# Kernel tuning notes

Hardware: AMD Instinct MI355X
Metric: run time of the kernel (lower is better)

The kernel has to match this reference:

```python
import jax, jax.numpy as jnp
import numpy as np

HEADS = 16
KEY_SIZE = 64
HEAD_SIZE = 64
D_MODEL = 1024
MASK_BIG = 1e12


def setup_inputs() -> dict:
    key = jax.random.key(0)
    ks = jax.random.split(key, 16)
    B, S, D = 4, 2048, D_MODEL
    qk_dim = HEADS * KEY_SIZE
    out_dim = HEADS * HEAD_SIZE
    s = 0.02
    return {
        'q': jax.random.normal(ks[0], (B, S, D), jnp.float32),
        'k': jax.random.normal(ks[1], (B, S, D), jnp.float32),
        'v': jax.random.normal(ks[2], (B, S, D), jnp.float32),
        'q_mask': jax.random.randint(ks[3], (B, S), 0, 2, jnp.int32),
        'v_mask': jax.random.randint(ks[4], (B, S), 0, 2, jnp.int32),
        'Wq': jax.random.normal(ks[5], (D, qk_dim), jnp.float32) * s,
        'bq': jnp.zeros((qk_dim,), jnp.float32),
        'Wk': jax.random.normal(ks[6], (D, qk_dim), jnp.float32) * s,
        'bk': jnp.zeros((qk_dim,), jnp.float32),
        'Wv': jax.random.normal(ks[7], (D, out_dim), jnp.float32) * s,
        'bv': jnp.zeros((out_dim,), jnp.float32),
        'Wo': jax.random.normal(ks[8], (out_dim, out_dim), jnp.float32) * s,
        'bo': jnp.zeros((out_dim,), jnp.float32),
    }


def reference(q, k, v, q_mask, v_mask, Wq, bq, Wk, bk, Wv, bv, Wo, bo):
    B, Sq, _ = q.shape
    Sk = k.shape[1]
    # projections -> [B, H, S, d]
    qw = (q @ Wq + bq).reshape(B, Sq, HEADS, KEY_SIZE).transpose(0, 2, 1, 3)
    kw = (k @ Wk + bk).reshape(B, Sk, HEADS, KEY_SIZE).transpose(0, 2, 1, 3)
    vw = (v @ Wv + bv).reshape(B, Sk, HEADS, HEAD_SIZE).transpose(0, 2, 1, 3)
    # scaled dot-product scores [B, H, Sq, Sk]
    a = jnp.einsum('bhqd,bhkd->bhqk', qw, kw) / np.sqrt(KEY_SIZE).astype(np.float32)
    # v_mask: additive -inf-like penalty on padded keys (mode=1, axis=-1)
    vm = v_mask.astype(a.dtype)[:, None, None, :]
    a = a - (1.0 - vm) * MASK_BIG
    # a_mask=True: causal mask (mask future positions)
    causal = jnp.tril(jnp.ones((Sq, Sk), a.dtype))
    a = a - (1.0 - causal) * MASK_BIG
    a = jax.nn.softmax(a, axis=-1)
    # attention output [B, Sq, H*head_size]
    o = jnp.einsum('bhqk,bhkd->bhqd', a, vw).transpose(0, 2, 1, 3).reshape(B, Sq, HEADS * HEAD_SIZE)
    o = o @ Wo + bo
    # q_mask: multiplicative zeroing of padded query outputs (mode=0, axis=1)
    o = o * q_mask.astype(o.dtype)[:, :, None]
    return o
```

## Files before the change

### kernel.cpp

```cpp
#include <hip/hip_runtime.h>
#include <hip/hip_bf16.h>

typedef __attribute__((ext_vector_type(8))) short v8s;
typedef __attribute__((ext_vector_type(4))) float v4f;
typedef __attribute__((ext_vector_type(16))) float v16f;
typedef __attribute__((ext_vector_type(4))) unsigned v4u;

#define S_LEN 2048
#define NB 4
#define NH 16
#define LOG2E 1.4426950408889634f
#define CMASK 1443109011456.0f
#define DEFER_THR 11.55f

__device__ __forceinline__ short f2bf(float f) {
    __hip_bfloat16 h = __float2bfloat16(f);
    union { __hip_bfloat16 h; short s; } u; u.h = h; return u.s;
}

__device__ __forceinline__ unsigned cvtpk(float lo, float hi) {
    unsigned r;
    asm("v_cvt_pk_bf16_f32 %0, %1, %2" : "=v"(r) : "v"(lo), "v"(hi));
    return r;
}

__device__ __forceinline__ void async16(void* lds, const void* g) {
    __builtin_amdgcn_global_load_lds(
        (const __attribute__((address_space(1))) unsigned int*)g,
        (__attribute__((address_space(3))) unsigned int*)lds, 16, 0, 0);
}

#define MFMA16(a, b, c) __builtin_amdgcn_mfma_f32_16x16x32_bf16((a), (b), (c), 0, 0, 0)
#define MFMA32(a, b, c) __builtin_amdgcn_mfma_f32_32x32x16_bf16((a), (b), (c), 0, 0, 0)

__global__ __launch_bounds__(256) void convert_all(const float* __restrict__ q,
                                                   const float* __restrict__ k,
                                                   const float* __restrict__ v,
                                                   short* __restrict__ Xq,
                                                   short* __restrict__ Xk,
                                                   short* __restrict__ Xv,
                                                   float* __restrict__ outz) {
    if (blockIdx.y == 3) {
        size_t i = ((size_t)blockIdx.x * 256 + threadIdx.x) * 8;
        float4 z4 = {0.f, 0.f, 0.f, 0.f};
        *(float4*)(outz + i) = z4;
        *(float4*)(outz + i + 4) = z4;
        return;
    }
    const float* in = (blockIdx.y == 0) ? q : (blockIdx.y == 1) ? k : v;
    short* out = (blockIdx.y == 0) ? Xq : (blockIdx.y == 1) ? Xk : Xv;
    size_t i = ((size_t)blockIdx.x * 256 + threadIdx.x) * 8;
    float4 a = *(const float4*)(in + i);
    float4 b = *(const float4*)(in + i + 4);
    v8s o;
    o[0] = f2bf(a.x); o[1] = f2bf(a.y); o[2] = f2bf(a.z); o[3] = f2bf(a.w);
    o[4] = f2bf(b.x); o[5] = f2bf(b.y); o[6] = f2bf(b.z); o[7] = f2bf(b.w);
    *(v8s*)(out + i) = o;
}

__global__ __launch_bounds__(256) void build_pen(const int* __restrict__ vm,
                                                 short* __restrict__ penC) {
    int i = blockIdx.x * 256 + threadIdx.x;
    penC[i] = vm[i] ? (short)0 : f2bf(-CMASK);
}

__global__ __launch_bounds__(256) void compact_qmask(const int* __restrict__ qm,
                                                     int* __restrict__ idx,
                                                     int* __restrict__ nq) {
    const int b = blockIdx.x;
    const int* m = qm + b * S_LEN;
    int* ib = idx + b * S_LEN;
    __shared__ int cnt[256];
    const int t = threadIdx.x;
    int loc[8], c = 0;
#pragma unroll
    for (int i = 0; i < 8; ++i) { int s = t * 8 + i; if (m[s]) loc[c++] = s; }
    cnt[t] = c;
    __syncthreads();
    for (int d = 1; d < 256; d <<= 1) {
        int v = (t >= d) ? cnt[t - d] : 0;
        __syncthreads();
        cnt[t] += v;
        __syncthreads();
    }
    int off = cnt[t] - c;
    for (int i = 0; i < c; ++i) ib[off + i] = loc[i];
    if (t == 255) nq[b] = cnt[255];
}

__global__ __launch_bounds__(256) void transpose_all(const float* __restrict__ Wq,
                                                     const float* __restrict__ Wk,
                                                     const float* __restrict__ Wv,
                                                     const float* __restrict__ Wo,
                                                     short* __restrict__ WTq,
                                                     short* __restrict__ WTk,
                                                     short* __restrict__ WTv,
                                                     short* __restrict__ WTo) {
    const int z = blockIdx.z;
    const float* W = (z == 0) ? Wq : (z == 1) ? Wk : (z == 2) ? Wv : Wo;
    short* WT = (z == 0) ? WTq : (z == 1) ? WTk : (z == 2) ? WTv : WTo;
    __shared__ float tile[32][33];
    int k0 = blockIdx.x * 32, n0 = blockIdx.y * 32;
    int tx = threadIdx.x & 31, ty = threadIdx.x >> 5;
#pragma unroll
    for (int i = 0; i < 4; ++i)
        tile[ty + i * 8][tx] = W[(size_t)(k0 + ty + i * 8) * 1024 + n0 + tx];
    __syncthreads();
#pragma unroll
    for (int i = 0; i < 4; ++i)
        WT[(size_t)(n0 + ty + i * 8) * 1024 + k0 + tx] = f2bf(tile[tx][ty + i * 8]);
}

__global__ __launch_bounds__(256)
void proj_all(const short* __restrict__ Xk, const short* __restrict__ Xv,
              const short* __restrict__ Xq,
              const short* __restrict__ WTk, const short* __restrict__ WTv,
              const short* __restrict__ WTq,
              const float* __restrict__ bk, const float* __restrict__ bv,
              const float* __restrict__ bq,
              const int* __restrict__ idx, const int* __restrict__ nq,
              short* __restrict__ KW, short* __restrict__ VT,
              short* __restrict__ QW) {
    __shared__ short As[128 * 64];
    __shared__ short Bs[128 * 64];
    const int tid = threadIdx.x;
    const int l = tid & 63, w = tid >> 6;
    const int g = l >> 4, ql = l & 15;
    const int z = blockIdx.z;
    const int n0 = blockIdx.x * 128;
    const int by = blockIdx.y;
    const int wr = w >> 1, wc = w & 1;

    int b = 0, m0 = by * 128, m0c = 0, nqv = 0;
    const int* idxb = nullptr;
    if (z == 2) {
        if (by >= 36) return;
        b = by / 9; m0c = (by % 9) * 128;
        nqv = nq[b];
        if (m0c >= nqv) return;
        idxb = idx + b * S_LEN;
    }
    const short* A  = (z == 0) ? Xk : (z == 1) ? Xv : Xq;
    const short* BT = (z == 0) ? WTk : (z == 1) ? WTv : WTq;
    const float* bias = (z == 0) ? bk : (z == 1) ? bv : bq;

    int arow[4];
#pragma unroll
    for (int i = 0; i < 4; ++i) {
        int row = (i * 256 + tid) >> 3;
        if (z == 2) {
            int jc = m0c + row;
            arow[i] = b * S_LEN + idxb[(jc < nqv) ? jc : (nqv - 1)];
        } else {
            arow[i] = m0 + row;
        }
    }
    const int c8 = (tid & 7) * 8;

    v4f acc[4][4] = {};

    for (int kt = 0; kt < 16; ++kt) {
        const int kk = kt * 64;
        __syncthreads();
#pragma unroll
        for (int i = 0; i < 4; ++i) {
            int ci = i * 256 + tid;
            async16((char*)As + (size_t)(i * 256 + w * 64) * 16,
                    A + (size_t)arow[i] * 1024 + kk + c8);
            async16((char*)Bs + (size_t)(i * 256 + w * 64) * 16,
                    BT + (size_t)(n0 + (ci >> 3)) * 1024 + kk + c8);
        }
        __syncthreads();
#pragma unroll
        for (int ks = 0; ks < 2; ++ks) {
            v8s af[4], bfr[4];
#pragma unroll
            for (int mt = 0; mt < 4; ++mt)
                af[mt] = *(const v8s*)(As + (wr * 64 + mt * 16 + ql) * 64 + ks * 32 + g * 8);
#pragma unroll
            for (int nt = 0; nt < 4; ++nt)
                bfr[nt] = *(const v8s*)(Bs + (wc * 64 + nt * 16 + ql) * 64 + ks * 32 + g * 8);
#pragma unroll
            for (int mt = 0; mt < 4; ++mt)
#pragma unroll
                for (int nt = 0; nt < 4; ++nt)
                    acc[mt][nt] = MFMA16(af[mt], bfr[nt], acc[mt][nt]);
        }
    }

#pragma unroll
    for (int nt = 0; nt < 4; ++nt) {
        int col = n0 + wc * 64 + nt * 16 + ql;
        float bval = bias[col];
        int hh = col >> 6, dd = col & 63;
#pragma unroll
        for (int mt = 0; mt < 4; ++mt) {
#pragma unroll
            for (int r = 0; r < 4; ++r) {
                int lrow = wr * 64 + mt * 16 + g * 4 + r;
                float vv = acc[mt][nt][r] + bval;
                if (z == 0) {
                    int gm = m0 + lrow;
                    int bb = gm >> 11, ss = gm & 2047;
                    KW[((size_t)(bb * NH + hh) * S_LEN + ss) * 64 + dd] = f2bf(vv);
                } else if (z == 1) {
                    int gm = m0 + lrow;
                    int bb = gm >> 11, ss = gm & 2047;
                    VT[((size_t)(bb * NH + hh) * 64 + dd) * S_LEN + ss] = f2bf(vv);
                } else {
                    int jc = m0c + lrow;
                    vv *= 0.125f * LOG2E;
                    QW[((size_t)(b * NH + hh) * S_LEN + jc) * 64 + dd] = f2bf(vv);
                }
            }
        }
    }
}

__global__ __launch_bounds__(64)
void attn_kernel(const short* __restrict__ QW, const short* __restrict__ KW,
                 const short* __restrict__ VT, const short* __restrict__ penC,
                 const int* __restrict__ idx, const int* __restrict__ nq,
                 short* __restrict__ O) {
    const int l = threadIdx.x;
    const int lq = l & 31, hi = l >> 5;
    const int bh = blockIdx.x;
    const int chunk = 63 - (int)blockIdx.y;
    const int b = bh >> 4, hd = bh & 15;

    const int nqv = nq[b];
    const int cy = chunk * 32;
    if (cy >= nqv) return;

    const short* Qp = QW + (size_t)bh * S_LEN * 64;
    const short* Kp = KW + (size_t)bh * S_LEN * 64;
    const short* Vp = VT + (size_t)bh * 64 * S_LEN;
    const short* pp = penC + b * S_LEN;
    const int* idxb = idx + b * S_LEN;

    const int j = cy + lq;
    const int jj = (j < nqv) ? j : (nqv - 1);
    const int q_glob = idxb[jj];
    const int qmin = __builtin_amdgcn_readfirstlane(q_glob);

    int lastj = cy + 31; if (lastj > nqv - 1) lastj = nqv - 1;
    const int NT = (idxb[lastj] >> 6) + 1;

    v8s qf[4];
#pragma unroll
    for (int ks = 0; ks < 4; ++ks)
        qf[ks] = *(const v8s*)(Qp + (size_t)jj * 64 + ks * 16 + hi * 8);
    v8s qf4 = {};
    qf4[0] = hi ? (short)0 : (short)0x3F80;

    v16f accO[2] = {};
    float m_run = -INFINITY, l_run = 0.f;

    auto tile = [&](int kt, bool causal) {
        const int k0 = kt * 64;
        const short* kb = Kp + (size_t)(k0 + lq) * 64 + hi * 8;
        const short* vb = Vp + (size_t)lq * S_LEN + k0 + hi * 8;
        short p0 = pp[k0 + lq], p1 = pp[k0 + lq + 32];

        v8s kf0[4], kf1[4];
#pragma unroll
        for (int ks = 0; ks < 4; ++ks) {
            kf0[ks] = *(const v8s*)(kb + ks * 16);
            kf1[ks] = *(const v8s*)(kb + 32 * 64 + ks * 16);
        }
        v16f acc0 = {}, acc1 = {};
        __builtin_amdgcn_s_setprio(1);
#pragma unroll
        for (int ks = 0; ks < 4; ++ks) {
            acc0 = MFMA32(kf0[ks], qf[ks], acc0);
            acc1 = MFMA32(kf1[ks], qf[ks], acc1);
        }
        v8s k4a = {}, k4b = {};
        k4a[0] = hi ? (short)0 : p0;
        k4b[0] = hi ? (short)0 : p1;
        acc0 = MFMA32(k4a, qf4, acc0);
        acc1 = MFMA32(k4b, qf4, acc1);
        __builtin_amdgcn_s_setprio(0);

        float s[32];
#pragma unroll
        for (int jn = 0; jn < 16; ++jn) { s[jn] = acc0[jn]; s[16 + jn] = acc1[jn]; }
        if (causal) {
#pragma unroll
            for (int t = 0; t < 2; ++t)
#pragma unroll
                for (int jn = 0; jn < 16; ++jn) {
                    int kp = k0 + t * 32 + (jn & 3) + 8 * (jn >> 2) + 4 * hi;
                    if (kp > q_glob) s[t * 16 + jn] -= CMASK;
                }
        }
        float t8[8];
#pragma unroll
        for (int i = 0; i < 8; ++i)
            t8[i] = fmaxf(fmaxf(s[i], s[i + 8]), fmaxf(s[i + 16], s[i + 24]));
#pragma unroll
        for (int i = 0; i < 4; ++i) t8[i] = fmaxf(t8[i], t8[i + 4]);
        float tmax = fmaxf(fmaxf(t8[0], t8[1]), fmaxf(t8[2], t8[3]));
        tmax = fmaxf(tmax, __shfl_xor(tmax, 32, 64));

        if (__any(tmax > m_run + DEFER_THR)) {
            float mnew = fmaxf(m_run, tmax);
            float scale = exp2f(m_run - mnew);
            m_run = mnew;
            l_run *= scale;
#pragma unroll
            for (int jn = 0; jn < 16; ++jn) {
                float sc = __shfl(scale, (jn & 3) + 8 * (jn >> 2) + 4 * hi, 64);
                accO[0][jn] *= sc;
                accO[1][jn] *= sc;
            }
        }
#pragma unroll
        for (int i = 0; i < 32; ++i) s[i] = exp2f(s[i] - m_run);
        float u8[8];
#pragma unroll
        for (int i = 0; i < 8; ++i)
            u8[i] = (s[i] + s[i + 8]) + (s[i + 16] + s[i + 24]);
#pragma unroll
        for (int i = 0; i < 4; ++i) u8[i] += u8[i + 4];
        float psum = (u8[0] + u8[1]) + (u8[2] + u8[3]);
        psum += __shfl_xor(psum, 32, 64);
        l_run += psum;

        v8s vf0[4], vf1[4];
#pragma unroll
        for (int ks = 0; ks < 4; ++ks) {
            vf0[ks] = *(const v8s*)(vb + ks * 16);
            vf1[ks] = *(const v8s*)(vb + 32 * S_LEN + ks * 16);
        }

        v8s PA[4];
#pragma unroll
        for (int t = 0; t < 2; ++t)
#pragma unroll
            for (int sf = 0; sf < 2; ++sf) {
                int base = t * 16 + sf * 8;
                unsigned x0 = cvtpk(s[base + 0], s[base + 1]);
                unsigned x1 = cvtpk(s[base + 2], s[base + 3]);
                unsigned y0 = cvtpk(s[base + 4], s[base + 5]);
                unsigned y1 = cvtpk(s[base + 6], s[base + 7]);
                asm volatile("v_permlane32_swap_b32 %0, %1" : "+v"(x0), "+v"(y0));
                asm volatile("v_permlane32_swap_b32 %0, %1" : "+v"(x1), "+v"(y1));
                v4u wv; wv[0] = x0; wv[1] = x1; wv[2] = y0; wv[3] = y1;
                union { v4u u; v8s s8; } cvt; cvt.u = wv;
                PA[t * 2 + sf] = cvt.s8;
            }

        __builtin_amdgcn_s_setprio(1);
#pragma unroll
        for (int ks = 0; ks < 4; ++ks) {
            accO[0] = MFMA32(PA[ks], vf0[ks], accO[0]);
            accO[1] = MFMA32(PA[ks], vf1[ks], accO[1]);
        }
        __builtin_amdgcn_s_setprio(0);
    };

    for (int kt = 0; kt < NT; ++kt)
        tile(kt, kt * 64 + 63 > qmin);

    int kt = NT;
    while (kt < 32 && __any(m_run < -1e11f)) {
        tile(kt, true);
        ++kt;
    }

    float inv = 1.0f / l_run;
#pragma unroll
    for (int jn = 0; jn < 16; ++jn) {
        int rowq = (jn & 3) + 8 * (jn >> 2) + 4 * hi;
        float iv = __shfl(inv, rowq, 64);
        int jrow = cy + rowq;
        if (jrow < nqv) {
            size_t base = (size_t)(b * S_LEN + jrow) * 1024 + hd * 64 + lq;
            O[base]      = f2bf(accO[0][jn] * iv);
            O[base + 32] = f2bf(accO[1][jn] * iv);
        }
    }
}

__global__ __launch_bounds__(256)
void out_gemm_c(const short* __restrict__ A, const short* __restrict__ BT,
                const float* __restrict__ bias, const int* __restrict__ idx,
                const int* __restrict__ nq, float* __restrict__ out) {
    __shared__ short As[128 * 64];
    __shared__ short Bs[128 * 64];
    const int tid = threadIdx.x;
    const int l = tid & 63, w = tid >> 6;
    const int g = l >> 4, ql = l & 15;
    const int n0 = blockIdx.x * 128;
    const int mb = blockIdx.y;
    const int b = mb / 9;
    const int m0c = (mb % 9) * 128;
    const int nqv = nq[b];
    if (m0c >= nqv) return;
    const int* idxb = idx + b * S_LEN;
    const int wr = w >> 1, wc = w & 1;

    v4f acc[4][4] = {};

    for (int kt = 0; kt < 16; ++kt) {
        const int kk = kt * 64;
        __syncthreads();
#pragma unroll
        for (int i = 0; i < 4; ++i) {
            int ci = i * 256 + tid;
            int row = ci >> 3, c = ci & 7;
            async16((char*)As + (size_t)(i * 256 + w * 64) * 16,
                    A + (size_t)(b * S_LEN + m0c + row) * 1024 + kk + c * 8);
            async16((char*)Bs + (size_t)(i * 256 + w * 64) * 16,
                    BT + (size_t)(n0 + row) * 1024 + kk + c * 8);
        }
        __syncthreads();
#pragma unroll
        for (int ks = 0; ks < 2; ++ks) {
            v8s af[4], bfr[4];
#pragma unroll
            for (int mt = 0; mt < 4; ++mt)
                af[mt] = *(const v8s*)(As + (wr * 64 + mt * 16 + ql) * 64 + ks * 32 + g * 8);
#pragma unroll
            for (int nt = 0; nt < 4; ++nt)
                bfr[nt] = *(const v8s*)(Bs + (wc * 64 + nt * 16 + ql) * 64 + ks * 32 + g * 8);
#pragma unroll
            for (int mt = 0; mt < 4; ++mt)
#pragma unroll
                for (int nt = 0; nt < 4; ++nt)
                    acc[mt][nt] = MFMA16(af[mt], bfr[nt], acc[mt][nt]);
        }
    }

#pragma unroll
    for (int nt = 0; nt < 4; ++nt) {
        int col = n0 + wc * 64 + nt * 16 + ql;
        float bval = bias[col];
#pragma unroll
        for (int mt = 0; mt < 4; ++mt) {
#pragma unroll
            for (int r = 0; r < 4; ++r) {
                int jc = m0c + wr * 64 + mt * 16 + g * 4 + r;
                if (jc < nqv) {
                    int orig = idxb[jc];
                    out[(size_t)(b * S_LEN + orig) * 1024 + col] =
                        acc[mt][nt][r] + bval;
                }
            }
        }
    }
}

extern "C" void kernel_launch(void* const* d_in, const int* in_sizes, int n_in,
                              void* d_out, int out_size, void* d_ws, size_t ws_size,
                              hipStream_t stream) {
    (void)in_sizes; (void)n_in; (void)out_size; (void)ws_size;
    const float* q  = (const float*)d_in[0];
    const float* k  = (const float*)d_in[1];
    const float* v  = (const float*)d_in[2];
    const int* qmask = (const int*)d_in[3];
    const int* vmask = (const int*)d_in[4];
    const float* Wq = (const float*)d_in[5];
    const float* bq = (const float*)d_in[6];
    const float* Wk = (const float*)d_in[7];
    const float* bk = (const float*)d_in[8];
    const float* Wv = (const float*)d_in[9];
    const float* bv = (const float*)d_in[10];
    const float* Wo = (const float*)d_in[11];
    const float* bo = (const float*)d_in[12];
    float* out = (float*)d_out;

    char* ws = (char*)d_ws;
    const size_t MB = 1024 * 1024;
    short* Xq  = (short*)(ws + 0 * MB);
    short* Xk  = (short*)(ws + 16 * MB);
    short* Xv  = (short*)(ws + 32 * MB);
    short* WTq = (short*)(ws + 48 * MB);
    short* WTk = (short*)(ws + 50 * MB);
    short* WTv = (short*)(ws + 52 * MB);
    short* WTo = (short*)(ws + 54 * MB);
    short* QW  = (short*)(ws + 56 * MB);
    short* KW  = (short*)(ws + 72 * MB);
    short* VTb = (short*)(ws + 88 * MB);
    short* Ob  = (short*)(ws + 104 * MB);
    short* penC = (short*)(ws + 120 * MB);
    int* idxB  = (int*)(ws + 121 * MB);
    int* nqB   = (int*)(ws + 122 * MB);

    convert_all<<<dim3(4096, 4), 256, 0, stream>>>(q, k, v, Xq, Xk, Xv, out);
    transpose_all<<<dim3(32, 32, 4), 256, 0, stream>>>(Wq, Wk, Wv, Wo,
                                                       WTq, WTk, WTv, WTo);
    build_pen<<<32, 256, 0, stream>>>(vmask, penC);
    compact_qmask<<<NB, 256, 0, stream>>>(qmask, idxB, nqB);

    proj_all<<<dim3(8, 64, 3), 256, 0, stream>>>(Xk, Xv, Xq, WTk, WTv, WTq,
                                                 bk, bv, bq, idxB, nqB,
                                                 KW, VTb, QW);
    attn_kernel<<<dim3(64, 64), 64, 0, stream>>>(QW, KW, VTb, penC, idxB, nqB, Ob);
    out_gemm_c<<<dim3(8, 36), 256, 0, stream>>>(Ob, WTo, bo, idxB, nqB, out);
}
```

Measured before the change: 262.2 us.

## Swizzle LDS tiles and remap GEMM block order for L2 locality

Applies an XOR swizzle to the LDS layout of the A and B tiles in the projection and output GEMMs. The global-to-LDS loads permute source columns so the MFMA fragment reads avoid bank conflicts. Blocks are also remapped from a 2D grid to a 1D grid grouped in 8x8 supertiles, so concurrent blocks share A and B tiles in L2. The output GEMM grid grows to 320 blocks, some of which exit early, which adds a little launch overhead.

```diff
diff --git a/kernel.cpp b/kernel.cpp
--- a/kernel.cpp
+++ b/kernel.cpp
@@ -22,6 +22,10 @@
     unsigned r;
     asm("v_cvt_pk_bf16_f32 %0, %1, %2" : "=v"(r) : "v"(lo), "v"(hi));
     return r;
+}
+
+__device__ __forceinline__ int swz(int row, int col) {
+    return (row * 128 + col) ^ ((row & 7) << 4);
 }
 
 __device__ __forceinline__ void async16(void* lds, const void* g) {
@@ -127,15 +131,16 @@
     const int l = tid & 63, w = tid >> 6;
     const int g = l >> 4, ql = l & 15;
     const int z = blockIdx.z;
-    const int n0 = blockIdx.x * 128;
-    const int by = blockIdx.y;
+    const int bid = blockIdx.x;
+    const int y = (bid & 7) + 8 * (bid >> 6);
+    const int n0 = ((bid >> 3) & 7) * 128;
     const int wr = w >> 1, wc = w & 1;
 
-    int b = 0, m0 = by * 128, m0c = 0, nqv = 0;
+    int b = 0, m0 = y * 128, m0c = 0, nqv = 0;
     const int* idxb = nullptr;
     if (z == 2) {
-        if (by >= 36) return;
-        b = by / 9; m0c = (by % 9) * 128;
+        if (y >= 36) return;
+        b = y / 9; m0c = (y % 9) * 128;
         nqv = nq[b];
         if (m0c >= nqv) return;
         idxb = idx + b * S_LEN;
@@ -155,7 +160,7 @@
             arow[i] = m0 + row;
         }
     }
-    const int c8 = (tid & 7) * 8;
+    const int c8 = (((l & 7) ^ (l >> 3))) * 8;
 
     v4f acc[4][4] = {};
 
@@ -176,10 +181,12 @@
             v8s af[4], bfr[4];
 #pragma unroll
             for (int mt = 0; mt < 4; ++mt)
-                af[mt] = *(const v8s*)(As + (wr * 64 + mt * 16 + ql) * 64 + ks * 32 + g * 8);
+                af[mt] = *(const v8s*)((char*)As +
+                          swz(wr * 64 + mt * 16 + ql, ks * 64 + g * 16));
 #pragma unroll
             for (int nt = 0; nt < 4; ++nt)
-                bfr[nt] = *(const v8s*)(Bs + (wc * 64 + nt * 16 + ql) * 64 + ks * 32 + g * 8);
+                bfr[nt] = *(const v8s*)((char*)Bs +
+                          swz(wc * 64 + nt * 16 + ql, ks * 64 + g * 16));
 #pragma unroll
             for (int mt = 0; mt < 4; ++mt)
 #pragma unroll
@@ -392,14 +399,17 @@
     const int tid = threadIdx.x;
     const int l = tid & 63, w = tid >> 6;
     const int g = l >> 4, ql = l & 15;
-    const int n0 = blockIdx.x * 128;
-    const int mb = blockIdx.y;
-    const int b = mb / 9;
-    const int m0c = (mb % 9) * 128;
+    const int bid = blockIdx.x;
+    const int y = (bid & 7) + 8 * (bid >> 6);
+    if (y >= 36) return;
+    const int n0 = ((bid >> 3) & 7) * 128;
+    const int b = y / 9;
+    const int m0c = (y % 9) * 128;
     const int nqv = nq[b];
     if (m0c >= nqv) return;
     const int* idxb = idx + b * S_LEN;
     const int wr = w >> 1, wc = w & 1;
+    const int c8 = (((l & 7) ^ (l >> 3))) * 8;
 
     v4f acc[4][4] = {};
 
@@ -409,11 +419,11 @@
 #pragma unroll
         for (int i = 0; i < 4; ++i) {
             int ci = i * 256 + tid;
-            int row = ci >> 3, c = ci & 7;
+            int row = ci >> 3;
             async16((char*)As + (size_t)(i * 256 + w * 64) * 16,
-                    A + (size_t)(b * S_LEN + m0c + row) * 1024 + kk + c * 8);
+                    A + (size_t)(b * S_LEN + m0c + row) * 1024 + kk + c8);
             async16((char*)Bs + (size_t)(i * 256 + w * 64) * 16,
-                    BT + (size_t)(n0 + row) * 1024 + kk + c * 8);
+                    BT + (size_t)(n0 + row) * 1024 + kk + c8);
         }
         __syncthreads();
 #pragma unroll
@@ -421,10 +431,12 @@
             v8s af[4], bfr[4];
 #pragma unroll
             for (int mt = 0; mt < 4; ++mt)
-                af[mt] = *(const v8s*)(As + (wr * 64 + mt * 16 + ql) * 64 + ks * 32 + g * 8);
+                af[mt] = *(const v8s*)((char*)As +
+                          swz(wr * 64 + mt * 16 + ql, ks * 64 + g * 16));
 #pragma unroll
             for (int nt = 0; nt < 4; ++nt)
-                bfr[nt] = *(const v8s*)(Bs + (wc * 64 + nt * 16 + ql) * 64 + ks * 32 + g * 8);
+                bfr[nt] = *(const v8s*)((char*)Bs +
+                          swz(wc * 64 + nt * 16 + ql, ks * 64 + g * 16));
 #pragma unroll
             for (int mt = 0; mt < 4; ++mt)
 #pragma unroll
@@ -494,9 +506,9 @@
     build_pen<<<32, 256, 0, stream>>>(vmask, penC);
     compact_qmask<<<NB, 256, 0, stream>>>(qmask, idxB, nqB);
 
-    proj_all<<<dim3(8, 64, 3), 256, 0, stream>>>(Xk, Xv, Xq, WTk, WTv, WTq,
-                                                 bk, bv, bq, idxB, nqB,
-                                                 KW, VTb, QW);
+    proj_all<<<dim3(512, 1, 3), 256, 0, stream>>>(Xk, Xv, Xq, WTk, WTv, WTq,
+                                                  bk, bv, bq, idxB, nqB,
+                                                  KW, VTb, QW);
     attn_kernel<<<dim3(64, 64), 64, 0, stream>>>(QW, KW, VTb, penC, idxB, nqB, Ob);
-    out_gemm_c<<<dim3(8, 36), 256, 0, stream>>>(Ob, WTo, bo, idxB, nqB, out);
-}
+    out_gemm_c<<<320, 256, 0, stream>>>(Ob, WTo, bo, idxB, nqB, out);
+}
```

After: 246.6 us. -5.9%, faster.
